# Performance work log

Hardware: AMD Instinct MI355X
Metric: run time of the kernel (lower is better)

The kernel has to match this reference:

```python
import jax, jax.numpy as jnp
import numpy as np

T, B, D, H = 1024, 64, 128, 256


def setup_inputs() -> dict:
    key = jax.random.key(0)
    ks = jax.random.split(key, 12)
    k = 1.0 / np.sqrt(H)  # torch LSTMCell init bound
    u = lambda kk, shape: jax.random.uniform(kk, shape, jnp.float32, -k, k)
    inputs = jax.random.normal(ks[0], (T, B, D), jnp.float32)
    hx = jnp.zeros((2, B, H), jnp.float32)
    cx = jnp.zeros((2, B, H), jnp.float32)
    return {
        'inputs': inputs, 'hx': hx, 'cx': cx,
        'Wih_f': u(ks[1], (4 * H, D)), 'Whh_f': u(ks[2], (4 * H, H)),
        'bih_f': u(ks[3], (4 * H,)), 'bhh_f': u(ks[4], (4 * H,)),
        'Wih_r': u(ks[5], (4 * H, D)), 'Whh_r': u(ks[6], (4 * H, H)),
        'bih_r': u(ks[7], (4 * H,)), 'bhh_r': u(ks[8], (4 * H,)),
    }


def _lstm_scan(x, h0, c0, Wih, Whh, bih, bhh, reverse):
    # Batch all input projections up front: [T,B,4H]
    gx = jnp.einsum('tbd,gd->tbg', x, Wih) + (bih + bhh)

    def step(carry, g):
        h, c = carry
        gates = g + h @ Whh.T  # [B,4H]
        i, f, gg, o = jnp.split(gates, 4, axis=-1)  # torch gate order i,f,g,o
        i = jax.nn.sigmoid(i)
        f = jax.nn.sigmoid(f)
        gg = jnp.tanh(gg)
        o = jax.nn.sigmoid(o)
        c = f * c + i * gg
        h = o * jnp.tanh(c)
        return (h, c), h

    # reverse=True scans back-to-front but emits outputs in original time
    # order, matching flip -> loop -> flip in the torch code.
    (h, c), ys = jax.lax.scan(step, (h0, c0), gx, reverse=reverse)
    return ys, h, c


def reference(inputs, hx, cx, Wih_f, Whh_f, bih_f, bhh_f,
              Wih_r, Whh_r, bih_r, bhh_r):
    yf, hf, cf = _lstm_scan(inputs, hx[0], cx[0], Wih_f, Whh_f, bih_f, bhh_f, False)
    yr, hr, cr = _lstm_scan(inputs, hx[1], cx[1], Wih_r, Whh_r, bih_r, bhh_r, True)
    out = jnp.concatenate([yf, yr], axis=-1)  # [T,B,2H]
    hy = jnp.stack([hf, hr], 0)  # [2,B,H]
    cy = jnp.stack([cf, cr], 0)
    return out, hy, cy
```

## Files before the change

kernel.cpp:

```cpp
#include <hip/hip_runtime.h>
#include <cstddef>

#define T_STEPS 1024
#define NB      64
#define DIN     128
#define HID     256
#define WPG     16

typedef unsigned short u16;
typedef unsigned int   u32;
typedef unsigned long long u64;
typedef __attribute__((ext_vector_type(8))) short short8;
typedef __attribute__((ext_vector_type(4))) float f32x4;

#define WG_OFF   0u
#define BIAS_OFF 1572864u
#define XB_OFF   1581056u
#define HB_OFF   18358272u
#define FL_OFF   18489344u

#define OUT_MAIN (T_STEPS * NB * 2 * HID)
#define TAIL_H   OUT_MAIN
#define TAIL_C   (OUT_MAIN + 2 * NB * HID)

__device__ __forceinline__ u16 f2bf(float f) {
  unsigned u = __float_as_uint(f);
  return (u16)((u + 0x7fffu + ((u >> 16) & 1u)) >> 16);
}
__device__ __forceinline__ float sigm(float v) { return 1.f / (1.f + __expf(-v)); }
__device__ __forceinline__ float tanh_fast(float x) {
  float e = __expf(-2.f * fabsf(x));
  float r = (1.f - e) / (1.f + e);
  return x < 0.f ? -r : r;
}

__global__ void prep_kernel(const float* __restrict__ x,
                            const float* __restrict__ Wih_f, const float* __restrict__ Whh_f,
                            const float* __restrict__ bih_f, const float* __restrict__ bhh_f,
                            const float* __restrict__ Wih_r, const float* __restrict__ Whh_r,
                            const float* __restrict__ bih_r, const float* __restrict__ bhh_r,
                            const float* __restrict__ hx,
                            u16* __restrict__ Wg, float* __restrict__ bias4,
                            u16* __restrict__ xb, u16* __restrict__ hbuf,
                            u32* __restrict__ flags) {
  const int total = 786432 + 2048 + 8388608 + 32768 + 128;
  for (int i = blockIdx.x * blockDim.x + threadIdx.x; i < total;
       i += gridDim.x * blockDim.x) {
    if (i < 786432) {
      int d = i / 393216;
      int r = i - d * 393216;
      int rowg = r / 384, k = r - rowg * 384;
      int j = rowg >> 2, q = rowg & 3;
      int g = q * HID + j;
      const float* Wih = d ? Wih_r : Wih_f;
      const float* Whh = d ? Whh_r : Whh_f;
      float v = (k < DIN) ? Wih[g * DIN + k] : Whh[g * HID + (k - DIN)];
      Wg[i] = f2bf(v);
    } else if (i < 786432 + 2048) {
      int r = i - 786432;
      int d = r >> 10, rowg = r & 1023;
      int j = rowg >> 2, q = rowg & 3;
      int g = q * HID + j;
      bias4[r] = d ? (bih_r[g] + bhh_r[g]) : (bih_f[g] + bhh_f[g]);
    } else if (i < 786432 + 2048 + 8388608) {
      int r = i - (786432 + 2048);
      xb[r] = f2bf(x[r]);
    } else if (i < 786432 + 2048 + 8388608 + 32768) {
      int r = i - (786432 + 2048 + 8388608);
      int d = r >> 14, b = (r >> 8) & 63, j = r & 255;
      int grp = d * 4 + (b >> 4), bb = b & 15;
      hbuf[((size_t)(8 + grp) * 16 + bb) * 256 + j] = f2bf(hx[r]);
      hbuf[((size_t)(0 + grp) * 16 + bb) * 256 + j] = 0;
    } else {
      flags[i - (786432 + 2048 + 8388608 + 32768)] = 0u;
    }
  }
}

#define MFMA __builtin_amdgcn_mfma_f32_16x16x32_bf16
#define ALD64(P) __hip_atomic_load((P), __ATOMIC_RELAXED, __HIP_MEMORY_SCOPE_AGENT)
#define MN2(F) { u32 a_ = (u32)(F), b_ = (u32)((F) >> 32); \
                 mn = mn < a_ ? mn : a_; mn = mn < b_ ? mn : b_; }

__global__ __launch_bounds__(256, 1) void lstm_r16(
    const u16* __restrict__ Wg, const float* __restrict__ bias4,
    const u16* __restrict__ xb, const float* __restrict__ cx,
    u16* __restrict__ hbuf, u32* __restrict__ flags,
    float* __restrict__ out) {
  extern __shared__ char smem[];
  u16* xsh  = (u16*)smem;
  u16* hsh  = (u16*)(smem + 8704);
  float* gl = (float*)(smem + 17152);

  const int tid = threadIdx.x;
  const int bid = blockIdx.x;
  const int grp = bid & 7;
  const int jsl = bid >> 3;
  const int d = grp >> 2, b0 = (grp & 3) * 16;
  const int w = tid >> 6, l = tid & 63;

  const u16* wgb = Wg + ((size_t)(d * 1024 + jsl * 64 + w * 16 + (l & 15))) * 384
                      + (l >> 4) * 8;
  short8 Wx0 = *(const short8*)(wgb + 0);
  short8 Wx1 = *(const short8*)(wgb + 32);
  short8 Wx2 = *(const short8*)(wgb + 64);
  short8 Wx3 = *(const short8*)(wgb + 96);
  short8 Wh0 = *(const short8*)(wgb + 128);
  short8 Wh1 = *(const short8*)(wgb + 160);
  short8 Wh2 = *(const short8*)(wgb + 192);
  short8 Wh3 = *(const short8*)(wgb + 224);
  short8 Wh4 = *(const short8*)(wgb + 256);
  short8 Wh5 = *(const short8*)(wgb + 288);
  short8 Wh6 = *(const short8*)(wgb + 320);
  short8 Wh7 = *(const short8*)(wgb + 352);
  const float bv = bias4[d * 1024 + jsl * 64 + w * 16 + (l & 15)];

  const int eb = tid >> 4, ej = tid & 15;
  const int jglob = jsl * 16 + ej;
  float c_reg = cx[((size_t)d * NB + b0 + eb) * HID + jglob];

  const int xr_row = tid >> 4;
  const int xc = (tid & 15) * 8;
  const int pb = tid >> 4;
  const int cj0 = (tid & 15) * 16;

  { int t0 = d ? 1023 : 0;
    *(uint4*)&xsh[(0 * 16 + xr_row) * 136 + xc] =
        *(const uint4*)&xb[((size_t)t0 * NB + b0 + xr_row) * DIN + xc]; }
  uint4 xv;
  { int t1 = d ? 1022 : 1;
    xv = *(const uint4*)&xb[((size_t)t1 * NB + b0 + xr_row) * DIN + xc]; }
  u64 h0, h1, h2, h3;
  { const u64* hp = (const u64*)(hbuf + ((size_t)(8 + grp) * 16 + pb) * 256 + cj0);
    h0 = ALD64(hp + 0); h1 = ALD64(hp + 1); h2 = ALD64(hp + 2); h3 = ALD64(hp + 3); }
  __syncthreads();

  f32x4 acc0 = {bv, bv, bv, bv}, acc1 = {0.f, 0.f, 0.f, 0.f};
  {
    const u16* xr = &xsh[(0 * 16 + (l & 15)) * 136 + (l >> 4) * 8];
    acc0 = MFMA(*(const short8*)(xr + 0),  Wx0, acc0, 0, 0, 0);
    acc1 = MFMA(*(const short8*)(xr + 32), Wx1, acc1, 0, 0, 0);
    acc0 = MFMA(*(const short8*)(xr + 64), Wx2, acc0, 0, 0, 0);
    acc1 = MFMA(*(const short8*)(xr + 96), Wx3, acc1, 0, 0, 0);
  }

  for (int s = 0; s < T_STEPS; ++s) {
    const int p = s & 1;
    const int t = d ? (1023 - s) : s;

    {
      uint4 H0, H1;
      H0.x = (u32)h0; H0.y = (u32)(h0 >> 32); H0.z = (u32)h1; H0.w = (u32)(h1 >> 32);
      H1.x = (u32)h2; H1.y = (u32)(h2 >> 32); H1.z = (u32)h3; H1.w = (u32)(h3 >> 32);
      *(uint4*)&hsh[pb * 264 + cj0] = H0;
      *(uint4*)&hsh[pb * 264 + cj0 + 8] = H1;
    }
    asm volatile("s_waitcnt lgkmcnt(0)" ::: "memory");
    __builtin_amdgcn_s_barrier();

    {
      const u16* hr = &hsh[(l & 15) * 264 + (l >> 4) * 8];
      acc0 = MFMA(*(const short8*)(hr + 0),   Wh0, acc0, 0, 0, 0);
      acc1 = MFMA(*(const short8*)(hr + 32),  Wh1, acc1, 0, 0, 0);
      acc0 = MFMA(*(const short8*)(hr + 64),  Wh2, acc0, 0, 0, 0);
      acc1 = MFMA(*(const short8*)(hr + 96),  Wh3, acc1, 0, 0, 0);
      acc0 = MFMA(*(const short8*)(hr + 128), Wh4, acc0, 0, 0, 0);
      acc1 = MFMA(*(const short8*)(hr + 160), Wh5, acc1, 0, 0, 0);
      acc0 = MFMA(*(const short8*)(hr + 192), Wh6, acc0, 0, 0, 0);
      acc1 = MFMA(*(const short8*)(hr + 224), Wh7, acc1, 0, 0, 0);
    }
    acc0 = acc0 + acc1;

    {
      int n = w * 16 + (l & 15);
      int m0 = (l >> 4) * 4;
      gl[(m0 + 0) * 68 + n] = acc0[0]; gl[(m0 + 1) * 68 + n] = acc0[1];
      gl[(m0 + 2) * 68 + n] = acc0[2]; gl[(m0 + 3) * 68 + n] = acc0[3];
    }
    asm volatile("s_waitcnt lgkmcnt(0)" ::: "memory");
    __builtin_amdgcn_s_barrier();

    float h, c;
    {
      f32x4 g4 = *(const f32x4*)&gl[eb * 68 + 4 * ej];
      float ii = sigm(g4[0]), ffg = sigm(g4[1]);
      float gg = tanh_fast(g4[2]), oo = sigm(g4[3]);
      c = ffg * c_reg + ii * gg;
      c_reg = c;
      h = oo * tanh_fast(c);
      __hip_atomic_store(hbuf + ((size_t)(p * 8 + grp) * 16 + eb) * 256 + jglob,
                         f2bf(h), __ATOMIC_RELAXED, __HIP_MEMORY_SCOPE_AGENT);
    }
    if (s < 1023) *(uint4*)&xsh[((p ^ 1) * 16 + xr_row) * 136 + xc] = xv;
    asm volatile("s_waitcnt vmcnt(0) lgkmcnt(0)" ::: "memory");
    __builtin_amdgcn_s_barrier();
    if (tid == 0 && s < 1023)
      __hip_atomic_store(flags + grp * WPG + jsl, (u32)(s + 1),
                         __ATOMIC_RELAXED, __HIP_MEMORY_SCOPE_AGENT);
    out[((size_t)t * NB + b0 + eb) * (2 * HID) + d * HID + jglob] = h;
    if (s == 1023) {
      out[TAIL_H + ((size_t)d * NB + b0 + eb) * HID + jglob] = h;
      out[TAIL_C + ((size_t)d * NB + b0 + eb) * HID + jglob] = c;
    }
    if (s < 1022) {
      int tn = d ? (1021 - s) : (s + 2);
      xv = *(const uint4*)&xb[((size_t)tn * NB + b0 + xr_row) * DIN + xc];
    }
    if (s < 1023) {
      acc0[0] = bv; acc0[1] = bv; acc0[2] = bv; acc0[3] = bv;
      acc1[0] = 0.f; acc1[1] = 0.f; acc1[2] = 0.f; acc1[3] = 0.f;
      {
        const u16* xr = &xsh[((p ^ 1) * 16 + (l & 15)) * 136 + (l >> 4) * 8];
        acc0 = MFMA(*(const short8*)(xr + 0),  Wx0, acc0, 0, 0, 0);
        acc1 = MFMA(*(const short8*)(xr + 32), Wx1, acc1, 0, 0, 0);
        acc0 = MFMA(*(const short8*)(xr + 64), Wx2, acc0, 0, 0, 0);
        acc1 = MFMA(*(const short8*)(xr + 96), Wx3, acc1, 0, 0, 0);
      }
      if (tid == 0) {
        const u64* fl = (const u64*)(flags + grp * WPG);
        const u32 want = (u32)(s + 1);
        while (1) {
          u64 f0 = ALD64(fl + 0), f1 = ALD64(fl + 1), f2 = ALD64(fl + 2), f3 = ALD64(fl + 3);
          u64 f4 = ALD64(fl + 4), f5 = ALD64(fl + 5), f6 = ALD64(fl + 6), f7 = ALD64(fl + 7);
          u32 mn = 0xffffffffu;
          MN2(f0) MN2(f1) MN2(f2) MN2(f3) MN2(f4) MN2(f5) MN2(f6) MN2(f7)
          if (mn >= want) break;
        }
      }
      __builtin_amdgcn_s_barrier();
      const u64* hp = (const u64*)(hbuf + ((size_t)(p * 8 + grp) * 16 + pb) * 256 + cj0);
      h0 = ALD64(hp + 0); h1 = ALD64(hp + 1); h2 = ALD64(hp + 2); h3 = ALD64(hp + 3);
    }
  }
}

extern "C" void kernel_launch(void* const* d_in, const int* in_sizes, int n_in,
                              void* d_out, int out_size, void* d_ws, size_t ws_size,
                              hipStream_t stream) {
  const float* x     = (const float*)d_in[0];
  const float* hx    = (const float*)d_in[1];
  const float* cx    = (const float*)d_in[2];
  const float* Wih_f = (const float*)d_in[3];
  const float* Whh_f = (const float*)d_in[4];
  const float* bih_f = (const float*)d_in[5];
  const float* bhh_f = (const float*)d_in[6];
  const float* Wih_r = (const float*)d_in[7];
  const float* Whh_r = (const float*)d_in[8];
  const float* bih_r = (const float*)d_in[9];
  const float* bhh_r = (const float*)d_in[10];
  float* out = (float*)d_out;

  u16* Wg      = (u16*)((char*)d_ws + WG_OFF);
  float* bias4 = (float*)((char*)d_ws + BIAS_OFF);
  u16* xb      = (u16*)((char*)d_ws + XB_OFF);
  u16* hbuf    = (u16*)((char*)d_ws + HB_OFF);
  u32* flags   = (u32*)((char*)d_ws + FL_OFF);

  hipFuncSetAttribute((const void*)lstm_r16,
                      hipFuncAttributeMaxDynamicSharedMemorySize, 86016);

  hipLaunchKernelGGL(prep_kernel, dim3(2048), dim3(256), 0, stream,
                     x, Wih_f, Whh_f, bih_f, bhh_f, Wih_r, Whh_r, bih_r, bhh_r,
                     hx, Wg, bias4, xb, hbuf, flags);
  hipLaunchKernelGGL(lstm_r16, dim3(128), dim3(256), 86016, stream,
                     Wg, bias4, xb, cx, hbuf, flags, out);
}
```

Baseline: 2.314 ms.

## Replace single-thread flag spin plus barrier with per-thread flag polling

Each thread now spins on one of the 16 producer flags of its group directly, instead of thread 0 polling all flags and then releasing the block with a barrier. The input-projection MFMAs move to the start of each step, after the x tile is staged into shared memory, and the lgkmcnt wait before the post-activation barrier is dropped. The aim is to take a barrier and the serial min-reduction off the critical path between timesteps. In exchange there are more concurrent atomic loads hammering the flag cache lines, and the x-projection MFMAs now sit on the dependent path instead of overlapping the wait. The shared-memory ordering of the x tile write versus its later read, now that the lgkm wait is gone, also needs care.

```diff
diff --git a/kernel.cpp b/kernel.cpp
--- a/kernel.cpp
+++ b/kernel.cpp
@@ -79,10 +79,9 @@
 
 #define MFMA __builtin_amdgcn_mfma_f32_16x16x32_bf16
 #define ALD64(P) __hip_atomic_load((P), __ATOMIC_RELAXED, __HIP_MEMORY_SCOPE_AGENT)
-#define MN2(F) { u32 a_ = (u32)(F), b_ = (u32)((F) >> 32); \
-                 mn = mn < a_ ? mn : a_; mn = mn < b_ ? mn : b_; }
-
-__global__ __launch_bounds__(256, 1) void lstm_r16(
+#define ALD32(P) __hip_atomic_load((P), __ATOMIC_RELAXED, __HIP_MEMORY_SCOPE_AGENT)
+
+__global__ __launch_bounds__(256, 1) void lstm_r18(
     const u16* __restrict__ Wg, const float* __restrict__ bias4,
     const u16* __restrict__ xb, const float* __restrict__ cx,
     u16* __restrict__ hbuf, u32* __restrict__ flags,
@@ -123,6 +122,7 @@
   const int xc = (tid & 15) * 8;
   const int pb = tid >> 4;
   const int cj0 = (tid & 15) * 16;
+  const u32* myflag = flags + grp * WPG + (tid & 15);
 
   { int t0 = d ? 1023 : 0;
     *(uint4*)&xsh[(0 * 16 + xr_row) * 136 + xc] =
@@ -135,19 +135,20 @@
     h0 = ALD64(hp + 0); h1 = ALD64(hp + 1); h2 = ALD64(hp + 2); h3 = ALD64(hp + 3); }
   __syncthreads();
 
-  f32x4 acc0 = {bv, bv, bv, bv}, acc1 = {0.f, 0.f, 0.f, 0.f};
-  {
-    const u16* xr = &xsh[(0 * 16 + (l & 15)) * 136 + (l >> 4) * 8];
-    acc0 = MFMA(*(const short8*)(xr + 0),  Wx0, acc0, 0, 0, 0);
-    acc1 = MFMA(*(const short8*)(xr + 32), Wx1, acc1, 0, 0, 0);
-    acc0 = MFMA(*(const short8*)(xr + 64), Wx2, acc0, 0, 0, 0);
-    acc1 = MFMA(*(const short8*)(xr + 96), Wx3, acc1, 0, 0, 0);
-  }
-
   for (int s = 0; s < T_STEPS; ++s) {
     const int p = s & 1;
     const int t = d ? (1023 - s) : s;
 
+    if (s < 1023) *(uint4*)&xsh[((p ^ 1) * 16 + xr_row) * 136 + xc] = xv;
+
+    f32x4 acc0 = {bv, bv, bv, bv}, acc1 = {0.f, 0.f, 0.f, 0.f};
+    {
+      const u16* xr = &xsh[(p * 16 + (l & 15)) * 136 + (l >> 4) * 8];
+      acc0 = MFMA(*(const short8*)(xr + 0),  Wx0, acc0, 0, 0, 0);
+      acc1 = MFMA(*(const short8*)(xr + 32), Wx1, acc1, 0, 0, 0);
+      acc0 = MFMA(*(const short8*)(xr + 64), Wx2, acc0, 0, 0, 0);
+      acc1 = MFMA(*(const short8*)(xr + 96), Wx3, acc1, 0, 0, 0);
+    }
     {
       uint4 H0, H1;
       H0.x = (u32)h0; H0.y = (u32)(h0 >> 32); H0.z = (u32)h1; H0.w = (u32)(h1 >> 32);
@@ -170,7 +171,6 @@
       acc1 = MFMA(*(const short8*)(hr + 224), Wh7, acc1, 0, 0, 0);
     }
     acc0 = acc0 + acc1;
-
     {
       int n = w * 16 + (l & 15);
       int m0 = (l >> 4) * 4;
@@ -180,19 +180,16 @@
     asm volatile("s_waitcnt lgkmcnt(0)" ::: "memory");
     __builtin_amdgcn_s_barrier();
 
-    float h, c;
-    {
-      f32x4 g4 = *(const f32x4*)&gl[eb * 68 + 4 * ej];
-      float ii = sigm(g4[0]), ffg = sigm(g4[1]);
-      float gg = tanh_fast(g4[2]), oo = sigm(g4[3]);
-      c = ffg * c_reg + ii * gg;
-      c_reg = c;
-      h = oo * tanh_fast(c);
-      __hip_atomic_store(hbuf + ((size_t)(p * 8 + grp) * 16 + eb) * 256 + jglob,
-                         f2bf(h), __ATOMIC_RELAXED, __HIP_MEMORY_SCOPE_AGENT);
-    }
-    if (s < 1023) *(uint4*)&xsh[((p ^ 1) * 16 + xr_row) * 136 + xc] = xv;
-    asm volatile("s_waitcnt vmcnt(0) lgkmcnt(0)" ::: "memory");
+    f32x4 g4 = *(const f32x4*)&gl[eb * 68 + 4 * ej];
+    float ii = sigm(g4[0]), ff = sigm(g4[1]);
+    float gg = tanh_fast(g4[2]), oo = sigm(g4[3]);
+    float c = ff * c_reg + ii * gg;
+    c_reg = c;
+    float h = oo * tanh_fast(c);
+    u16 hb16 = f2bf(h);
+    __hip_atomic_store(hbuf + ((size_t)(p * 8 + grp) * 16 + eb) * 256 + jglob,
+                       hb16, __ATOMIC_RELAXED, __HIP_MEMORY_SCOPE_AGENT);
+    asm volatile("s_waitcnt vmcnt(0)" ::: "memory");
     __builtin_amdgcn_s_barrier();
     if (tid == 0 && s < 1023)
       __hip_atomic_store(flags + grp * WPG + jsl, (u32)(s + 1),
@@ -207,27 +204,8 @@
       xv = *(const uint4*)&xb[((size_t)tn * NB + b0 + xr_row) * DIN + xc];
     }
     if (s < 1023) {
-      acc0[0] = bv; acc0[1] = bv; acc0[2] = bv; acc0[3] = bv;
-      acc1[0] = 0.f; acc1[1] = 0.f; acc1[2] = 0.f; acc1[3] = 0.f;
-      {
-        const u16* xr = &xsh[((p ^ 1) * 16 + (l & 15)) * 136 + (l >> 4) * 8];
-        acc0 = MFMA(*(const short8*)(xr + 0),  Wx0, acc0, 0, 0, 0);
-        acc1 = MFMA(*(const short8*)(xr + 32), Wx1, acc1, 0, 0, 0);
-        acc0 = MFMA(*(const short8*)(xr + 64), Wx2, acc0, 0, 0, 0);
-        acc1 = MFMA(*(const short8*)(xr + 96), Wx3, acc1, 0, 0, 0);
-      }
-      if (tid == 0) {
-        const u64* fl = (const u64*)(flags + grp * WPG);
-        const u32 want = (u32)(s + 1);
-        while (1) {
-          u64 f0 = ALD64(fl + 0), f1 = ALD64(fl + 1), f2 = ALD64(fl + 2), f3 = ALD64(fl + 3);
-          u64 f4 = ALD64(fl + 4), f5 = ALD64(fl + 5), f6 = ALD64(fl + 6), f7 = ALD64(fl + 7);
-          u32 mn = 0xffffffffu;
-          MN2(f0) MN2(f1) MN2(f2) MN2(f3) MN2(f4) MN2(f5) MN2(f6) MN2(f7)
-          if (mn >= want) break;
-        }
-      }
-      __builtin_amdgcn_s_barrier();
+      const u32 want = (u32)(s + 1);
+      while (ALD32(myflag) < want) { }
       const u64* hp = (const u64*)(hbuf + ((size_t)(p * 8 + grp) * 16 + pb) * 256 + cj0);
       h0 = ALD64(hp + 0); h1 = ALD64(hp + 1); h2 = ALD64(hp + 2); h3 = ALD64(hp + 3);
     }
@@ -256,12 +234,12 @@
   u16* hbuf    = (u16*)((char*)d_ws + HB_OFF);
   u32* flags   = (u32*)((char*)d_ws + FL_OFF);
 
-  hipFuncSetAttribute((const void*)lstm_r16,
+  hipFuncSetAttribute((const void*)lstm_r18,
                       hipFuncAttributeMaxDynamicSharedMemorySize, 86016);
 
   hipLaunchKernelGGL(prep_kernel, dim3(2048), dim3(256), 0, stream,
                      x, Wih_f, Whh_f, bih_f, bhh_f, Wih_r, Whh_r, bih_r, bhh_r,
                      hx, Wg, bias4, xb, hbuf, flags);
-  hipLaunchKernelGGL(lstm_r16, dim3(128), dim3(256), 86016, stream,
+  hipLaunchKernelGGL(lstm_r18, dim3(128), dim3(256), 86016, stream,
                      Wg, bias4, xb, cx, hbuf, flags, out);
 }
```

Measured after the change: 2.430 ms. 1.05x slower.
